# Kernel optimization log

Hardware: AMD Instinct MI355X
Metric: run time of the kernel (lower is better)

## Reference

```python
import jax, jax.numpy as jnp
import numpy as np

N, E, T = 20000, 320000, 64
INP, EMB, OUT = 128, 16, 3
HEADS, MSIZE, MDIM, KDIM, VDIM = 4, 1024, 128, 64, 64


def setup_inputs() -> dict:
    key = jax.random.key(0)
    ks = iter(jax.random.split(key, 64))

    def nrm(shape, s=0.05):
        return jax.random.normal(next(ks), shape, dtype=jnp.float32) * s

    return dict(
        x=jax.random.normal(next(ks), (N, INP), dtype=jnp.float32),
        edge_index=jax.random.randint(next(ks), (2, E), 0, N),
        index=5,
        inp_types=jax.random.randint(next(ks), (T,), 0, 4),
        log_return=jax.random.normal(next(ks), (T,), dtype=jnp.float32),
        # SAGEConv 1 (SoftmaxAggregation temp t1, lin_l/lin_r, bias=False)
        t1=jnp.ones((1, INP), jnp.float32),
        W1l=nrm((INP, 512)), W1r=nrm((INP, 512)),
        ln1g_w=jnp.ones((512,), jnp.float32), ln1g_b=jnp.zeros((512,), jnp.float32),
        # SAGEConv 2
        t2=jnp.ones((1, 512), jnp.float32),
        W2l=nrm((512, 256)), W2r=nrm((512, 256)),
        ln2g_w=jnp.ones((256,), jnp.float32), ln2g_b=jnp.zeros((256,), jnp.float32),
        # MemPooling(256,128,heads=4,num_clusters=1)
        mp_k=nrm((HEADS, 1, 256), 1.0),
        mp_conv=nrm((HEADS,), 0.5),            # Conv2d(heads,1,1,bias=False)
        mp_lin=nrm((256, 128)),                # Linear(in,out,bias=False)
        fxg_w=nrm((128, 256)), fxg_b=jnp.zeros((256,), jnp.float32),
        # PolicyNet head
        emb=nrm((4, EMB), 1.0),
        fk_w=nrm((256, KDIM)), fk_b=jnp.zeros((KDIM,), jnp.float32),
        fv_w=nrm((256, VDIM)), fv_b=jnp.zeros((VDIM,), jnp.float32),
        # MultiHeadMemory
        mem=nrm((HEADS, MSIZE, MDIM), 1.0),
        mfk_w=nrm((MDIM, KDIM)), mfk_b=jnp.zeros((KDIM,), jnp.float32),
        mfv_w=nrm((MDIM, VDIM)), mfv_b=jnp.zeros((VDIM,), jnp.float32),
        mfx_w=nrm((VDIM * HEADS, VDIM)), mfx_b=jnp.zeros((VDIM,), jnp.float32),
        f1_w=nrm((INP + EMB + 2 * VDIM + 1, 512)),
        n1_w=jnp.ones((512,), jnp.float32), n1_b=jnp.zeros((512,), jnp.float32),
        f2_w=nrm((512, 256)),
        n2_w=jnp.ones((256,), jnp.float32), n2_b=jnp.zeros((256,), jnp.float32),
        f3_w=nrm((256, OUT)), f3_b=jnp.zeros((OUT,), jnp.float32),
    )


def _forward(x, t1, W1l, W1r, ln1g_w, ln1g_b, t2, W2l, W2r, ln2g_w, ln2g_b,
             mp_k, mp_conv, mp_lin, fxg_w, fxg_b, emb, fk_w, fk_b, fv_w, fv_b,
             mem, mfk_w, mfk_b, mfv_w, mfv_b, mfx_w, mfx_b,
             f1_w, n1_w, n1_b, f2_w, n2_w, n2_b, f3_w, f3_b,
             log_return, edge_index, inp_types, index):
    n = x.shape[0]
    src, dst = edge_index[0], edge_index[1]

    def sage(h, t, Wl, Wr):
        hj = h[src]                                    # [E, C] gather
        gate = hj * t                                  # learned softmax temperature
        m = jax.ops.segment_max(gate, dst, num_segments=n)
        e = jnp.exp(gate - m[dst])                     # segment-stable softmax
        s = jax.ops.segment_sum(e, dst, num_segments=n)
        agg = jax.ops.segment_sum(hj * (e / s[dst]), dst, num_segments=n)
        return agg @ Wl + h @ Wr                       # SAGEConv, bias=False

    def graph_ln(h, w, b, eps=1e-5):                   # PyG LayerNorm, mode='graph'
        hc = h - jnp.mean(h)
        return hc / jnp.sqrt(jnp.mean(hc * hc) + eps) * w + b

    h = jax.nn.relu(graph_ln(sage(x, t1, W1l, W1r), ln1g_w, ln1g_b))
    h = jax.nn.relu(graph_ln(sage(h, t2, W2l, W2r), ln2g_w, ln2g_b))

    # MemPooling (single graph => B=1), tau=1: student-t kernel over sq. distances
    H, K, C = mp_k.shape
    kk = mp_k.reshape(H * K, C)
    d2 = jnp.maximum(jnp.sum(kk * kk, 1)[:, None] - 2.0 * (kk @ h.T)
                     + jnp.sum(h * h, 1)[None, :], 0.0)        # [H*K, N]
    dist = 1.0 / (1.0 + d2)
    dist = dist.reshape(H, K, n).transpose(0, 2, 1)[None]      # [1, H, N, K]
    S = dist / jnp.sum(dist, -1, keepdims=True)
    S = jax.nn.softmax(jnp.einsum('h,bhnk->bnk', mp_conv, S), axis=-1)  # [1, N, K]
    zp = jnp.einsum('bnk,nc->bkc', S, h)[:, 0, :]              # squeeze(1), K==1
    z = (zp @ mp_lin) @ fxg_w + fxg_b                          # [1, 256]

    q = jax.nn.softmax(z @ fk_w + fk_b, axis=-1)               # [1, key_dim]
    v = z @ fv_w + fv_b                                        # [1, val_dim]

    # MultiHeadMemory
    km = jax.nn.softmax(mem @ mfk_w + mfk_b, axis=-1)          # [H, M, key]
    vm = mem @ mfv_w + mfv_b                                   # [H, M, val]
    w = jax.nn.softmax(jnp.einsum('bk,hnk->bhn', q, km), axis=-1)
    mv = jnp.einsum('bhn,hnv->bhv', w, vm).reshape(q.shape[0], -1)
    m_out = mv @ mfx_w + mfx_b                                 # [1, val]

    zz = jnp.concatenate([v, m_out], axis=-1)                  # [1, 2*val]
    t_len = inp_types.shape[0]
    xi = jnp.broadcast_to(x[index][None, :], (t_len, x.shape[1]))
    zb = jnp.broadcast_to(zz, (t_len, zz.shape[1]))
    feat = jnp.concatenate([xi, emb[inp_types], log_return.reshape(-1, 1), zb], axis=-1)

    def ln(h2, w2, b2, eps=1e-5):                              # nn.LayerNorm (last dim)
        mu = jnp.mean(h2, -1, keepdims=True)
        hc = h2 - mu
        return hc / jnp.sqrt(jnp.mean(hc * hc, -1, keepdims=True) + eps) * w2 + b2

    h1 = jax.nn.relu(ln(feat @ f1_w, n1_w, n1_b))              # dropout = identity (eval)
    h2 = jax.nn.relu(ln(h1 @ f2_w, n2_w, n2_b))
    return jax.nn.softmax(h2 @ f3_w + f3_b, axis=-1)           # [T, out_dim]


def reference(x, edge_index, index, inp_types, log_return, t1, W1l, W1r, ln1g_w, ln1g_b,
              t2, W2l, W2r, ln2g_w, ln2g_b, mp_k, mp_conv, mp_lin, fxg_w, fxg_b, emb,
              fk_w, fk_b, fv_w, fv_b, mem, mfk_w, mfk_b, mfv_w, mfv_b, mfx_w, mfx_b,
              f1_w, n1_w, n1_b, f2_w, n2_w, n2_b, f3_w, f3_b):
    return _forward(x, t1, W1l, W1r, ln1g_w, ln1g_b, t2, W2l, W2r, ln2g_w, ln2g_b,
                    mp_k, mp_conv, mp_lin, fxg_w, fxg_b, emb, fk_w, fk_b, fv_w, fv_b,
                    mem, mfk_w, mfk_b, mfv_w, mfv_b, mfx_w, mfx_b,
                    f1_w, n1_w, n1_b, f2_w, n2_w, n2_b, f3_w, f3_b,
                    log_return, edge_index, inp_types, index)
```

## Files before the change

### kernel.cpp

```cpp
#include <hip/hip_runtime.h>

typedef __attribute__((ext_vector_type(8))) short bf16x8;
typedef __attribute__((ext_vector_type(8))) unsigned short ushort8_t;
typedef __attribute__((ext_vector_type(4))) float f32x4;

__device__ __forceinline__ unsigned short f2bf(float f) {
    unsigned int x = __float_as_uint(f);
    unsigned int r = x + 0x7fffu + ((x >> 16) & 1u);
    return (unsigned short)(r >> 16);
}
__device__ __forceinline__ float bf2f(unsigned short u) {
    return __uint_as_float(((unsigned int)u) << 16);
}
__device__ __forceinline__ float fexp2(float x) { return __builtin_amdgcn_exp2f(x); }

#define LOG2E 1.44269504089f

__global__ void count_kernel(const int* __restrict__ dst, int E, int* __restrict__ counts) {
    int i = blockIdx.x * 256 + threadIdx.x;
    if (i < E) atomicAdd(&counts[dst[i]], 1);
}

template <int CHUNK>
__global__ __launch_bounds__(1024) void scan_kernel(int* __restrict__ cnt,
                                                    int* __restrict__ off, int n) {
    __shared__ int s[1024];
    int tid = threadIdx.x;
    int base = tid * CHUNK;
    int loc[CHUNK];
    int sum = 0;
#pragma unroll
    for (int i = 0; i < CHUNK; ++i) {
        int idx = base + i;
        int v = 0;
        if (idx < n) { v = cnt[idx]; cnt[idx] = 0; }
        sum += v;
        loc[i] = sum;
    }
    s[tid] = sum;
    __syncthreads();
    for (int d = 1; d < 1024; d <<= 1) {
        int t = (tid >= d) ? s[tid - d] : 0;
        __syncthreads();
        s[tid] += t;
        __syncthreads();
    }
    int prev = (tid > 0) ? s[tid - 1] : 0;
    if (tid == 0) off[0] = 0;
#pragma unroll
    for (int i = 0; i < CHUNK; ++i) {
        int idx = base + i;
        if (idx < n) off[idx + 1] = prev + loc[i];
    }
}

__global__ void fill_kernel(const int* __restrict__ src, const int* __restrict__ dst, int E,
                            const int* __restrict__ off, int* __restrict__ cursor,
                            int* __restrict__ srcs) {
    int i = blockIdx.x * 256 + threadIdx.x;
    if (i < E) {
        int d = dst[i];
        int p = atomicAdd(&cursor[d], 1);
        srcs[off[d] + p] = src[i];
    }
}

__global__ __launch_bounds__(256) void cast_bf16(const float* __restrict__ in,
                                                 unsigned short* __restrict__ out, size_t n) {
    size_t stride = (size_t)gridDim.x * 256 * 4;
    for (size_t i = ((size_t)blockIdx.x * 256 + threadIdx.x) * 4; i < n; i += stride) {
        float4 v = *(const float4*)(in + i);
        ushort4 o;
        o.x = f2bf(v.x); o.y = f2bf(v.y); o.z = f2bf(v.z); o.w = f2bf(v.w);
        *(ushort4*)(out + i) = o;
    }
}

__global__ __launch_bounds__(256) void agg512(const unsigned short* __restrict__ h,
                                              const float* __restrict__ t,
                                              const int* __restrict__ off,
                                              const int* __restrict__ srcs,
                                              unsigned short* __restrict__ agg, int n) {
    int wid = threadIdx.x >> 6, lane = threadIdx.x & 63;
    int node = blockIdx.x * 4 + wid;
    if (node >= n) return;
    int beg = off[node], end = off[node + 1];
    int col = lane * 8;
    float tc[8], sE[8], sW[8];
#pragma unroll
    for (int i = 0; i < 8; ++i) { tc[i] = t[col + i] * LOG2E; sE[i] = 0.f; sW[i] = 0.f; }
#define P8(u)                                       \
    _Pragma("unroll") for (int i = 0; i < 8; ++i) { \
        float v = bf2f(u[i]);                       \
        float wv = fexp2(v * tc[i]);                \
        sE[i] += wv; sW[i] += v * wv;               \
    }
    int e = beg;
    for (; e + 2 <= end; e += 2) {
        int s0 = srcs[e], s1 = srcs[e + 1];
        ushort8_t u0 = *(const ushort8_t*)(h + (size_t)s0 * 512 + col);
        ushort8_t u1 = *(const ushort8_t*)(h + (size_t)s1 * 512 + col);
        P8(u0) P8(u1)
    }
    if (e < end) {
        int s0 = srcs[e];
        ushort8_t u0 = *(const ushort8_t*)(h + (size_t)s0 * 512 + col);
        P8(u0)
    }
#undef P8
    ushort8_t o;
#pragma unroll
    for (int i = 0; i < 8; ++i) o[i] = f2bf((end > beg) ? (sW[i] / sE[i]) : 0.f);
    *(ushort8_t*)(agg + (size_t)node * 512 + col) = o;
}

__global__ __launch_bounds__(256) void agg128(const unsigned short* __restrict__ h,
                                              const float* __restrict__ t,
                                              const int* __restrict__ off,
                                              const int* __restrict__ srcs,
                                              unsigned short* __restrict__ agg, int n) {
    int wid = threadIdx.x >> 6, lane = threadIdx.x & 63;
    int node = blockIdx.x * 4 + wid;
    if (node >= n) return;
    int beg = off[node], end = off[node + 1];
    int col = lane * 2;
    float t0 = t[col] * LOG2E, t1 = t[col + 1] * LOG2E;
    float e0 = 0.f, e1 = 0.f, w0 = 0.f, w1 = 0.f;
#define P2(u)                                          \
    {                                                  \
        float a = bf2f(u.x), b = bf2f(u.y);            \
        float xa = fexp2(a * t0), xb = fexp2(b * t1);  \
        e0 += xa; e1 += xb; w0 += a * xa; w1 += b * xb; \
    }
    int e = beg;
    for (; e + 4 <= end; e += 4) {
        ushort2 u0 = *(const ushort2*)(h + (size_t)srcs[e] * 128 + col);
        ushort2 u1 = *(const ushort2*)(h + (size_t)srcs[e + 1] * 128 + col);
        ushort2 u2 = *(const ushort2*)(h + (size_t)srcs[e + 2] * 128 + col);
        ushort2 u3 = *(const ushort2*)(h + (size_t)srcs[e + 3] * 128 + col);
        P2(u0) P2(u1) P2(u2) P2(u3)
    }
    for (; e < end; ++e) {
        ushort2 u0 = *(const ushort2*)(h + (size_t)srcs[e] * 128 + col);
        P2(u0)
    }
#undef P2
    ushort2 o;
    o.x = f2bf((end > beg) ? (w0 / e0) : 0.f);
    o.y = f2bf((end > beg) ? (w1 / e1) : 0.f);
    *(ushort2*)(agg + (size_t)node * 128 + col) = o;
}

__global__ void pack_w(const float* __restrict__ Wl, const float* __restrict__ Wr,
                       int K1, int K2, int N, unsigned short* __restrict__ Bt) {
    int idx = blockIdx.x * 256 + threadIdx.x;
    int Kc = K1 + K2;
    if (idx < N * Kc) {
        int n = idx / Kc;
        int k = idx - n * Kc;
        float v = (k < K1) ? Wl[(size_t)k * N + n] : Wr[(size_t)(k - K1) * N + n];
        Bt[idx] = f2bf(v);
    }
}

__global__ __launch_bounds__(512) void gemm_dual_mfma2(
    const unsigned short* __restrict__ A1, const unsigned short* __restrict__ A2,
    const unsigned short* __restrict__ Bt,
    unsigned short* __restrict__ Cb, double* __restrict__ part,
    int M, int N, int K1, int K2) {
    const int Kc = K1 + K2;
    __shared__ unsigned short As[128 * 40];
    __shared__ unsigned short Bs[256 * 40];
    __shared__ double rs[512], rs2[512];
    int tid = threadIdx.x;
    int lane = tid & 63, w = tid >> 6;
    int wm = w & 1, wn = w >> 1;
    int m0 = blockIdx.y * 128, n0 = blockIdx.x * 256;
    f32x4 acc[4][4] = {};
    int kg = lane >> 4, lr = lane & 15;

    for (int k0 = 0; k0 < Kc; k0 += 32) {
        const unsigned short* Asrc;
        int kk, Ksrc;
        if (k0 < K1) { Asrc = A1; kk = k0; Ksrc = K1; }
        else         { Asrc = A2; kk = k0 - K1; Ksrc = K2; }
        {
            int r = tid >> 2, ch = tid & 3;
            int gr = m0 + r;
            ushort8_t v = {0, 0, 0, 0, 0, 0, 0, 0};
            if (gr < M) v = *(const ushort8_t*)(Asrc + (size_t)gr * Ksrc + kk + ch * 8);
            *(ushort8_t*)&As[r * 40 + ch * 8] = v;
        }
#pragma unroll
        for (int it = 0; it < 2; ++it) {
            int idx = tid + it * 512;
            int r = idx >> 2, ch = idx & 3;
            const unsigned short* srcp = Bt + (size_t)(n0 + r) * Kc + k0 + ch * 8;
            *(ushort8_t*)&Bs[r * 40 + ch * 8] = *(const ushort8_t*)srcp;
        }
        __syncthreads();
        bf16x8 a[4], b[4];
#pragma unroll
        for (int i = 0; i < 4; ++i)
            a[i] = *(bf16x8*)&As[(wm * 64 + i * 16 + lr) * 40 + kg * 8];
#pragma unroll
        for (int j = 0; j < 4; ++j)
            b[j] = *(bf16x8*)&Bs[(wn * 64 + j * 16 + lr) * 40 + kg * 8];
#pragma unroll
        for (int i = 0; i < 4; ++i)
#pragma unroll
            for (int j = 0; j < 4; ++j)
                acc[i][j] = __builtin_amdgcn_mfma_f32_16x16x32_bf16(a[i], b[j], acc[i][j], 0, 0, 0);
        __syncthreads();
    }
    double s = 0, s2 = 0;
#pragma unroll
    for (int i = 0; i < 4; ++i) {
        int rbase = m0 + wm * 64 + i * 16 + kg * 4;
#pragma unroll
        for (int j = 0; j < 4; ++j) {
            int col = n0 + wn * 64 + j * 16 + lr;
#pragma unroll
            for (int reg = 0; reg < 4; ++reg) {
                int row = rbase + reg;
                if (row < M) {
                    float v = acc[i][j][reg];
                    Cb[(size_t)row * N + col] = f2bf(v);
                    s += v;
                    s2 += (double)v * v;
                }
            }
        }
    }
    rs[tid] = s;
    rs2[tid] = s2;
    __syncthreads();
    for (int d = 256; d; d >>= 1) {
        if (tid < d) { rs[tid] += rs[tid + d]; rs2[tid] += rs2[tid + d]; }
        __syncthreads();
    }
    if (tid == 0) {
        int bid = blockIdx.y * gridDim.x + blockIdx.x;
        part[bid * 2] = rs[0];
        part[bid * 2 + 1] = rs2[0];
    }
}

template <int C>
__global__ __launch_bounds__(256) void ln_relu_ip(unsigned short* __restrict__ z,
                                                  const float* __restrict__ w,
                                                  const float* __restrict__ b,
                                                  const double* __restrict__ part, int nb,
                                                  float invn, size_t n) {
    __shared__ float st[2];
    if (threadIdx.x < 64) {
        double s = 0, s2 = 0;
        for (int i = threadIdx.x; i < nb; i += 64) { s += part[2 * i]; s2 += part[2 * i + 1]; }
        for (int d = 32; d; d >>= 1) { s += __shfl_down(s, d); s2 += __shfl_down(s2, d); }
        if (threadIdx.x == 0) {
            float mu = (float)(s * invn);
            float var = (float)(s2 * invn) - mu * mu;
            st[0] = mu;
            st[1] = rsqrtf(var + 1e-5f);
        }
    }
    __syncthreads();
    float mu = st[0], inv = st[1];
    size_t stride = (size_t)gridDim.x * 256 * 4;
    for (size_t i = ((size_t)blockIdx.x * 256 + threadIdx.x) * 4; i < n; i += stride) {
        ushort4 v = *(const ushort4*)(z + i);
        int c = (int)(i & (C - 1));
        ushort4 o;
        o.x = f2bf(fmaxf((bf2f(v.x) - mu) * inv * w[c] + b[c], 0.f));
        o.y = f2bf(fmaxf((bf2f(v.y) - mu) * inv * w[c + 1] + b[c + 1], 0.f));
        o.z = f2bf(fmaxf((bf2f(v.z) - mu) * inv * w[c + 2] + b[c + 2], 0.f));
        o.w = f2bf(fmaxf((bf2f(v.w) - mu) * inv * w[c + 3] + b[c + 3], 0.f));
        *(ushort4*)(z + i) = o;
    }
}

__global__ __launch_bounds__(256) void colsum_t(const unsigned short* __restrict__ h2,
                                                float* __restrict__ cspartT, int n) {
    __shared__ float red[8 * 256];
    int tid = threadIdx.x;
    int cg = tid & 31;
    int rl = tid >> 5;
    int rows_per = (n + gridDim.x - 1) / gridDim.x;
    int r0 = blockIdx.x * rows_per;
    int r1 = min(n, r0 + rows_per);
    int c8 = cg * 8;
    float acc[8] = {};
    for (int r = r0 + rl; r < r1; r += 8) {
        ushort8_t u = *(const ushort8_t*)(h2 + (size_t)r * 256 + c8);
#pragma unroll
        for (int i = 0; i < 8; ++i) acc[i] += bf2f(u[i]);
    }
#pragma unroll
    for (int i = 0; i < 8; ++i) red[rl * 256 + c8 + i] = acc[i];
    __syncthreads();
    float s = 0;
#pragma unroll
    for (int r = 0; r < 8; ++r) s += red[r * 256 + tid];
    cspartT[tid * 64 + blockIdx.x] = s;
}

__global__ __launch_bounds__(256) void zqv_kernel(const float* __restrict__ cspartT,
                                                  const float* __restrict__ mp_lin,
                                                  const float* __restrict__ fxg_w,
                                                  const float* __restrict__ fxg_b,
                                                  const float* __restrict__ fk_w,
                                                  const float* __restrict__ fk_b,
                                                  const float* __restrict__ fv_w,
                                                  const float* __restrict__ fv_b,
                                                  float* __restrict__ qv) {
    __shared__ float zp_s[256], u_s[128], z_s[256], ql_s[64];
    __shared__ float part_s[1024];
    int tid = threadIdx.x;
    {
        float s = 0;
        const float* p = cspartT + tid * 64;
#pragma unroll
        for (int i = 0; i < 16; ++i) {
            float4 v = *(const float4*)(p + i * 4);
            s += v.x + v.y + v.z + v.w;
        }
        zp_s[tid] = s;
    }
    __syncthreads();
    {
        int og = tid & 31, kc = tid >> 5;
        int j4 = og * 4;
        f32x4 a = {0.f, 0.f, 0.f, 0.f};
        for (int ci = 0; ci < 32; ++ci) {
            int c = kc * 32 + ci;
            float4 w = *(const float4*)(mp_lin + (size_t)c * 128 + j4);
            float zc = zp_s[c];
            a[0] += zc * w.x; a[1] += zc * w.y; a[2] += zc * w.z; a[3] += zc * w.w;
        }
#pragma unroll
        for (int i = 0; i < 4; ++i) part_s[kc * 128 + j4 + i] = a[i];
    }
    __syncthreads();
    if (tid < 128) {
        float s = 0;
#pragma unroll
        for (int kc = 0; kc < 8; ++kc) s += part_s[kc * 128 + tid];
        u_s[tid] = s;
    }
    __syncthreads();
    {
        int og = tid & 63, kc = tid >> 6;
        int j4 = og * 4;
        f32x4 a = {0.f, 0.f, 0.f, 0.f};
        for (int ci = 0; ci < 32; ++ci) {
            int c = kc * 32 + ci;
            float4 w = *(const float4*)(fxg_w + (size_t)c * 256 + j4);
            float uc = u_s[c];
            a[0] += uc * w.x; a[1] += uc * w.y; a[2] += uc * w.z; a[3] += uc * w.w;
        }
#pragma unroll
        for (int i = 0; i < 4; ++i) part_s[kc * 256 + j4 + i] = a[i];
    }
    __syncthreads();
    {
        float s = fxg_b[tid];
#pragma unroll
        for (int kc = 0; kc < 4; ++kc) s += part_s[kc * 256 + tid];
        z_s[tid] = s;
    }
    __syncthreads();
    {
        int og = tid & 15, kc = tid >> 4;
        int j4 = og * 4;
        f32x4 a = {0.f, 0.f, 0.f, 0.f};
        for (int ci = 0; ci < 16; ++ci) {
            int c = kc * 16 + ci;
            float4 w = *(const float4*)(fk_w + (size_t)c * 64 + j4);
            float zc = z_s[c];
            a[0] += zc * w.x; a[1] += zc * w.y; a[2] += zc * w.z; a[3] += zc * w.w;
        }
#pragma unroll
        for (int i = 0; i < 4; ++i) part_s[kc * 64 + j4 + i] = a[i];
    }
    __syncthreads();
    if (tid < 64) {
        float s = fk_b[tid];
#pragma unroll
        for (int kc = 0; kc < 16; ++kc) s += part_s[kc * 64 + tid];
        ql_s[tid] = s;
    }
    __syncthreads();
    {
        int og = tid & 15, kc = tid >> 4;
        int j4 = og * 4;
        f32x4 a = {0.f, 0.f, 0.f, 0.f};
        for (int ci = 0; ci < 16; ++ci) {
            int c = kc * 16 + ci;
            float4 w = *(const float4*)(fv_w + (size_t)c * 64 + j4);
            float zc = z_s[c];
            a[0] += zc * w.x; a[1] += zc * w.y; a[2] += zc * w.z; a[3] += zc * w.w;
        }
#pragma unroll
        for (int i = 0; i < 4; ++i) part_s[kc * 64 + j4 + i] = a[i];
    }
    __syncthreads();
    if (tid < 64) {
        float mx = ql_s[tid];
        for (int d = 32; d; d >>= 1) mx = fmaxf(mx, __shfl_xor(mx, d));
        float e = __expf(ql_s[tid] - mx);
        float s = e;
        for (int d = 32; d; d >>= 1) s += __shfl_xor(s, d);
        qv[tid] = e / s;
        float vv = fv_b[tid];
#pragma unroll
        for (int kc = 0; kc < 16; ++kc) vv += part_s[kc * 64 + tid];
        qv[64 + tid] = vv;
    }
}

__global__ __launch_bounds__(256) void mem_kv_logit(const float* __restrict__ mem,
                                                    const float* __restrict__ mfk_w,
                                                    const float* __restrict__ mfk_b,
                                                    const float* __restrict__ mfv_w,
                                                    const float* __restrict__ mfv_b,
                                                    const float* __restrict__ qv,
                                                    float* __restrict__ logits,
                                                    float* __restrict__ vm) {
    __shared__ float rows[4][128];
    __shared__ float qs[64];
    int tid = threadIdx.x;
    int r0 = blockIdx.x * 4;
    if (tid < 64) qs[tid] = qv[tid];
    for (int i = tid; i < 512; i += 256) rows[i >> 7][i & 127] = mem[(size_t)r0 * 128 + i];
    __syncthreads();
    int lr = tid >> 6;
    int lane = tid & 63;
    const float* row = rows[lr];
    float kl = mfk_b[lane], vl = mfv_b[lane];
#pragma unroll 8
    for (int c = 0; c < 128; ++c) {
        float rv = row[c];
        kl += rv * mfk_w[c * 64 + lane];
        vl += rv * mfv_w[c * 64 + lane];
    }
    float mx = kl;
    for (int d = 32; d; d >>= 1) mx = fmaxf(mx, __shfl_xor(mx, d));
    float e = __expf(kl - mx);
    float s = e;
    for (int d = 32; d; d >>= 1) s += __shfl_xor(s, d);
    float kval = e / s;
    float wl = kval * qs[lane];
    for (int d = 32; d; d >>= 1) wl += __shfl_xor(wl, d);
    size_t gr = (size_t)(r0 + lr);
    if (lane == 0) logits[gr] = wl;
    vm[gr * 64 + lane] = vl;
}

__global__ __launch_bounds__(256) void attend_part(const float* __restrict__ logits,
                                                   const float* __restrict__ vm,
                                                   float* __restrict__ part) {
    int b = blockIdx.x;
    int h = b >> 4;
    int s0 = (b & 15) * 64;
    int tid = threadIdx.x;
    __shared__ float els[64];
    __shared__ float pr[4][64];
    __shared__ float lmax_s, lsum_s;
    if (tid < 64) {
        float lg = logits[h * 1024 + s0 + tid];
        float m = lg;
        for (int d = 32; d; d >>= 1) m = fmaxf(m, __shfl_xor(m, d));
        float e = __expf(lg - m);
        els[tid] = e;
        float s = e;
        for (int d = 32; d; d >>= 1) s += __shfl_xor(s, d);
        if (tid == 0) { lmax_s = m; lsum_s = s; }
    }
    __syncthreads();
    int dd = tid & 63, g = tid >> 6;
    float acc = 0;
    for (int s = g; s < 64; s += 4)
        acc += els[s] * vm[((size_t)h * 1024 + s0 + s) * 64 + dd];
    pr[g][dd] = acc;
    __syncthreads();
    if (tid < 64) {
        float pv = pr[0][tid] + pr[1][tid] + pr[2][tid] + pr[3][tid];
        part[b * 66 + 2 + tid] = pv;
        if (tid == 0) { part[b * 66] = lmax_s; part[b * 66 + 1] = lsum_s; }
    }
}

__global__ __launch_bounds__(256) void attend_final(const float* __restrict__ part,
                                                    const float* __restrict__ mfx_w,
                                                    const float* __restrict__ mfx_b,
                                                    float* __restrict__ m_out) {
    __shared__ float mv[256];
    __shared__ float part_s[1024];
    int tid = threadIdx.x;
    int h = tid >> 6, dd = tid & 63;
    float gmax = -1e30f;
#pragma unroll
    for (int p = 0; p < 16; ++p) gmax = fmaxf(gmax, part[(h * 16 + p) * 66]);
    float total = 0.f, acc = 0.f;
#pragma unroll
    for (int p = 0; p < 16; ++p) {
        float sc = __expf(part[(h * 16 + p) * 66] - gmax);
        total += part[(h * 16 + p) * 66 + 1] * sc;
        acc += part[(h * 16 + p) * 66 + 2 + dd] * sc;
    }
    mv[h * 64 + dd] = acc / total;
    __syncthreads();
    {
        int og = tid & 15, kc = tid >> 4;
        int j4 = og * 4;
        f32x4 a = {0.f, 0.f, 0.f, 0.f};
        for (int ci = 0; ci < 16; ++ci) {
            int c = kc * 16 + ci;
            float4 w = *(const float4*)(mfx_w + (size_t)c * 64 + j4);
            float mc = mv[c];
            a[0] += mc * w.x; a[1] += mc * w.y; a[2] += mc * w.z; a[3] += mc * w.w;
        }
#pragma unroll
        for (int i = 0; i < 4; ++i) part_s[kc * 64 + j4 + i] = a[i];
    }
    __syncthreads();
    if (tid < 64) {
        float s = mfx_b[tid];
#pragma unroll
        for (int kc = 0; kc < 16; ++kc) s += part_s[kc * 64 + tid];
        m_out[tid] = s;
    }
}

__device__ __forceinline__ float block_sum_256(float v, float* red) {
    int tid = threadIdx.x;
    red[tid] = v;
    __syncthreads();
    for (int d = 128; d; d >>= 1) { if (tid < d) red[tid] += red[tid + d]; __syncthreads(); }
    float r = red[0];
    __syncthreads();
    return r;
}

__global__ __launch_bounds__(256) void head_kernel(
    const float* __restrict__ x, const int* __restrict__ index_p,
    const int* __restrict__ inp_types, const float* __restrict__ log_return,
    const float* __restrict__ emb, const float* __restrict__ qv,
    const float* __restrict__ m_out, const float* __restrict__ f1_w,
    const float* __restrict__ n1_w, const float* __restrict__ n1_b,
    const float* __restrict__ f2_w, const float* __restrict__ n2_w,
    const float* __restrict__ n2_b, const float* __restrict__ f3_w,
    const float* __restrict__ f3_b, float* __restrict__ out) {
    __shared__ float feat[273];
    __shared__ float h1[512];
    __shared__ float h2[256];
    __shared__ float red[256];
    __shared__ float l3[3];
    int r = blockIdx.x, tid = threadIdx.x;
    int idx = index_p[0];
    for (int i = tid; i < 273; i += 256) {
        float val;
        if (i < 128) val = x[(size_t)idx * 128 + i];
        else if (i < 144) val = emb[inp_types[r] * 16 + (i - 128)];
        else if (i == 144) val = log_return[r];
        else if (i < 209) val = qv[64 + (i - 145)];
        else val = m_out[i - 209];
        feat[i] = val;
    }
    __syncthreads();
    float a0 = 0, a1 = 0;
    for (int c = 0; c < 273; ++c) {
        float f = feat[c];
        a0 += f * f1_w[c * 512 + tid];
        a1 += f * f1_w[c * 512 + tid + 256];
    }
    float mu = block_sum_256(a0 + a1, red) / 512.f;
    float c0 = a0 - mu, c1 = a1 - mu;
    float var = block_sum_256(c0 * c0 + c1 * c1, red) / 512.f;
    float inv = rsqrtf(var + 1e-5f);
    h1[tid] = fmaxf(c0 * inv * n1_w[tid] + n1_b[tid], 0.f);
    h1[tid + 256] = fmaxf(c1 * inv * n1_w[tid + 256] + n1_b[tid + 256], 0.f);
    __syncthreads();
    float b0 = 0;
    for (int c = 0; c < 512; ++c) b0 += h1[c] * f2_w[c * 256 + tid];
    float mu2 = block_sum_256(b0, red) / 256.f;
    float cc = b0 - mu2;
    float var2 = block_sum_256(cc * cc, red) / 256.f;
    float inv2 = rsqrtf(var2 + 1e-5f);
    h2[tid] = fmaxf(cc * inv2 * n2_w[tid] + n2_b[tid], 0.f);
    __syncthreads();
    if (tid < 3) {
        float a = f3_b[tid];
        for (int c = 0; c < 256; ++c) a += h2[c] * f3_w[c * 3 + tid];
        l3[tid] = a;
    }
    __syncthreads();
    if (tid < 3) {
        float mx = fmaxf(l3[0], fmaxf(l3[1], l3[2]));
        float s = __expf(l3[0] - mx) + __expf(l3[1] - mx) + __expf(l3[2] - mx);
        out[r * 3 + tid] = __expf(l3[tid] - mx) / s;
    }
}

extern "C" void kernel_launch(void* const* d_in, const int* in_sizes, int n_in,
                              void* d_out, int out_size, void* d_ws, size_t ws_size,
                              hipStream_t stream) {
    const float* x = (const float*)d_in[0];
    const int* ei = (const int*)d_in[1];
    const int* index_p = (const int*)d_in[2];
    const int* inp_types = (const int*)d_in[3];
    const float* log_return = (const float*)d_in[4];
    const float* t1 = (const float*)d_in[5];
    const float* W1l = (const float*)d_in[6];
    const float* W1r = (const float*)d_in[7];
    const float* ln1g_w = (const float*)d_in[8];
    const float* ln1g_b = (const float*)d_in[9];
    const float* t2 = (const float*)d_in[10];
    const float* W2l = (const float*)d_in[11];
    const float* W2r = (const float*)d_in[12];
    const float* ln2g_w = (const float*)d_in[13];
    const float* ln2g_b = (const float*)d_in[14];
    const float* mp_lin = (const float*)d_in[17];
    const float* fxg_w = (const float*)d_in[18];
    const float* fxg_b = (const float*)d_in[19];
    const float* emb = (const float*)d_in[20];
    const float* fk_w = (const float*)d_in[21];
    const float* fk_b = (const float*)d_in[22];
    const float* fv_w = (const float*)d_in[23];
    const float* fv_b = (const float*)d_in[24];
    const float* mem = (const float*)d_in[25];
    const float* mfk_w = (const float*)d_in[26];
    const float* mfk_b = (const float*)d_in[27];
    const float* mfv_w = (const float*)d_in[28];
    const float* mfv_b = (const float*)d_in[29];
    const float* mfx_w = (const float*)d_in[30];
    const float* mfx_b = (const float*)d_in[31];
    const float* f1_w = (const float*)d_in[32];
    const float* n1_w = (const float*)d_in[33];
    const float* n1_b = (const float*)d_in[34];
    const float* f2_w = (const float*)d_in[35];
    const float* n2_w = (const float*)d_in[36];
    const float* n2_b = (const float*)d_in[37];
    const float* f3_w = (const float*)d_in[38];
    const float* f3_b = (const float*)d_in[39];
    float* out = (float*)d_out;

    int n = in_sizes[0] / 128;
    int E = in_sizes[1] / 2;
    int T = in_sizes[3];
    const int* src = ei;
    const int* dst = ei + E;

    char* w = (char*)d_ws;
    auto alloc = [&](size_t bytes) {
        char* p = w;
        w += (bytes + 255) & ~(size_t)255;
        return p;
    };
    int* counts = (int*)alloc((size_t)n * 4);
    int* off = (int*)alloc((size_t)(n + 1) * 4);
    int* srcs = (int*)alloc((size_t)E * 4);
    unsigned short* xb = (unsigned short*)alloc((size_t)n * 128 * 2);
    unsigned short* agg1b = (unsigned short*)alloc((size_t)n * 128 * 2);
    unsigned short* z1b = (unsigned short*)alloc((size_t)n * 512 * 2);
    unsigned short* agg2b = (unsigned short*)alloc((size_t)n * 512 * 2);
    unsigned short* z2b = (unsigned short*)alloc((size_t)n * 256 * 2);
    double* partd = (double*)alloc(1024 * 2 * 8);
    float* cspartT = (float*)alloc(256 * 64 * 4);
    float* qv = (float*)alloc(128 * 4);
    float* logits = (float*)alloc((size_t)4 * 1024 * 4);
    float* vm = (float*)alloc((size_t)4 * 1024 * 64 * 4);
    float* apart = (float*)alloc(64 * 66 * 4);
    float* m_out = (float*)alloc(64 * 4);
    unsigned short* Bt1 = (unsigned short*)alloc((size_t)512 * 256 * 2);
    unsigned short* Bt2 = (unsigned short*)alloc((size_t)256 * 1024 * 2);

    int nblk_e = (E + 255) / 256;
    int mblk = (n + 127) / 128;

    hipMemsetAsync(counts, 0, (size_t)n * 4, stream);
    count_kernel<<<nblk_e, 256, 0, stream>>>(dst, E, counts);
    scan_kernel<20><<<1, 1024, 0, stream>>>(counts, off, n);
    fill_kernel<<<nblk_e, 256, 0, stream>>>(src, dst, E, off, counts, srcs);

    pack_w<<<(512 * 256 + 255) / 256, 256, 0, stream>>>(W1l, W1r, 128, 128, 512, Bt1);
    pack_w<<<(256 * 1024 + 255) / 256, 256, 0, stream>>>(W2l, W2r, 512, 512, 256, Bt2);
    cast_bf16<<<1024, 256, 0, stream>>>(x, xb, (size_t)n * 128);

    agg128<<<(n + 3) / 4, 256, 0, stream>>>(xb, t1, off, srcs, agg1b, n);
    gemm_dual_mfma2<<<dim3(2, mblk), 512, 0, stream>>>(agg1b, xb, Bt1, z1b, partd, n, 512, 128, 128);
    ln_relu_ip<512><<<1024, 256, 0, stream>>>(z1b, ln1g_w, ln1g_b, partd, 2 * mblk,
                                              1.0f / ((float)n * 512.f), (size_t)n * 512);

    agg512<<<(n + 3) / 4, 256, 0, stream>>>(z1b, t2, off, srcs, agg2b, n);
    gemm_dual_mfma2<<<dim3(1, mblk), 512, 0, stream>>>(agg2b, z1b, Bt2, z2b, partd, n, 256, 512, 512);
    ln_relu_ip<256><<<512, 256, 0, stream>>>(z2b, ln2g_w, ln2g_b, partd, mblk,
                                             1.0f / ((float)n * 256.f), (size_t)n * 256);

    colsum_t<<<64, 256, 0, stream>>>(z2b, cspartT, n);
    zqv_kernel<<<1, 256, 0, stream>>>(cspartT, mp_lin, fxg_w, fxg_b, fk_w, fk_b, fv_w, fv_b, qv);

    mem_kv_logit<<<1024, 256, 0, stream>>>(mem, mfk_w, mfk_b, mfv_w, mfv_b, qv, logits, vm);
    attend_part<<<64, 256, 0, stream>>>(logits, vm, apart);
    attend_final<<<1, 256, 0, stream>>>(apart, mfx_w, mfx_b, m_out);

    head_kernel<<<T, 256, 0, stream>>>(x, index_p, inp_types, log_return, emb, qv, m_out,
                                       f1_w, n1_w, n1_b, f2_w, n2_w, n2_b, f3_w, f3_b, out);
}
```

Before: 300.7 us.

## Fuse preprocessing kernels and fold final LayerNorm-ReLU into column sum

Merges the edge-count, x-to-bf16 cast and both weight-packing kernels into one prep kernel launched over the edge grid. It also removes the in-place LayerNorm+ReLU pass over z2 and applies the normalization and ReLU on the fly inside the column-sum reduction. Only the column sums are consumed downstream, so the separate read-modify-write of z2 is dropped. The cost is fewer launches and less memory traffic, in exchange for a prep kernel that has more work per thread and no bf16 rounding of the normalized values before summation.

After: 290.1 us. 3.5% less time.

```diff
diff --git a/kernel.cpp b/kernel.cpp
--- a/kernel.cpp
+++ b/kernel.cpp
@@ -16,9 +16,30 @@
 
 #define LOG2E 1.44269504089f
 
-__global__ void count_kernel(const int* __restrict__ dst, int E, int* __restrict__ counts) {
+__global__ __launch_bounds__(256) void prep_kernel(
+    const int* __restrict__ dst, int E, int* __restrict__ counts,
+    const float* __restrict__ x, unsigned short* __restrict__ xb, size_t nx4,
+    const float* __restrict__ W1l, const float* __restrict__ W1r, unsigned short* __restrict__ Bt1,
+    const float* __restrict__ W2l, const float* __restrict__ W2r, unsigned short* __restrict__ Bt2) {
     int i = blockIdx.x * 256 + threadIdx.x;
+    int total = gridDim.x * 256;
     if (i < E) atomicAdd(&counts[dst[i]], 1);
+    for (size_t j = i; j < nx4; j += total) {
+        float4 v = *(const float4*)(x + j * 4);
+        ushort4 o;
+        o.x = f2bf(v.x); o.y = f2bf(v.y); o.z = f2bf(v.z); o.w = f2bf(v.w);
+        *(ushort4*)(xb + j * 4) = o;
+    }
+    if (i < 512 * 256) {
+        int nn = i >> 8, k = i & 255;
+        float v = (k < 128) ? W1l[(size_t)k * 512 + nn] : W1r[(size_t)(k - 128) * 512 + nn];
+        Bt1[i] = f2bf(v);
+    }
+    if (i < 256 * 1024) {
+        int nn = i >> 10, k = i & 1023;
+        float v = (k < 512) ? W2l[(size_t)k * 256 + nn] : W2r[(size_t)(k - 512) * 256 + nn];
+        Bt2[i] = f2bf(v);
+    }
 }
 
 template <int CHUNK>
@@ -62,17 +83,6 @@
         int d = dst[i];
         int p = atomicAdd(&cursor[d], 1);
         srcs[off[d] + p] = src[i];
-    }
-}
-
-__global__ __launch_bounds__(256) void cast_bf16(const float* __restrict__ in,
-                                                 unsigned short* __restrict__ out, size_t n) {
-    size_t stride = (size_t)gridDim.x * 256 * 4;
-    for (size_t i = ((size_t)blockIdx.x * 256 + threadIdx.x) * 4; i < n; i += stride) {
-        float4 v = *(const float4*)(in + i);
-        ushort4 o;
-        o.x = f2bf(v.x); o.y = f2bf(v.y); o.z = f2bf(v.z); o.w = f2bf(v.w);
-        *(ushort4*)(out + i) = o;
     }
 }
 
@@ -151,18 +161,6 @@
     *(ushort2*)(agg + (size_t)node * 128 + col) = o;
 }
 
-__global__ void pack_w(const float* __restrict__ Wl, const float* __restrict__ Wr,
-                       int K1, int K2, int N, unsigned short* __restrict__ Bt) {
-    int idx = blockIdx.x * 256 + threadIdx.x;
-    int Kc = K1 + K2;
-    if (idx < N * Kc) {
-        int n = idx / Kc;
-        int k = idx - n * Kc;
-        float v = (k < K1) ? Wl[(size_t)k * N + n] : Wr[(size_t)(k - K1) * N + n];
-        Bt[idx] = f2bf(v);
-    }
-}
-
 __global__ __launch_bounds__(512) void gemm_dual_mfma2(
     const unsigned short* __restrict__ A1, const unsigned short* __restrict__ A2,
     const unsigned short* __restrict__ Bt,
@@ -279,21 +277,42 @@
     }
 }
 
-__global__ __launch_bounds__(256) void colsum_t(const unsigned short* __restrict__ h2,
-                                                float* __restrict__ cspartT, int n) {
+__global__ __launch_bounds__(256) void ln_colsum(const unsigned short* __restrict__ z2,
+                                                 const float* __restrict__ w,
+                                                 const float* __restrict__ b,
+                                                 const double* __restrict__ part, int nb,
+                                                 float invn, int n,
+                                                 float* __restrict__ cspartT) {
     __shared__ float red[8 * 256];
+    __shared__ float st[2];
     int tid = threadIdx.x;
+    if (tid < 64) {
+        double s = 0, s2 = 0;
+        for (int i = tid; i < nb; i += 64) { s += part[2 * i]; s2 += part[2 * i + 1]; }
+        for (int d = 32; d; d >>= 1) { s += __shfl_down(s, d); s2 += __shfl_down(s2, d); }
+        if (tid == 0) {
+            float mu = (float)(s * invn);
+            float var = (float)(s2 * invn) - mu * mu;
+            st[0] = mu;
+            st[1] = rsqrtf(var + 1e-5f);
+        }
+    }
+    __syncthreads();
+    float mu = st[0], inv = st[1];
     int cg = tid & 31;
     int rl = tid >> 5;
+    int c8 = cg * 8;
+    float lw[8], lb[8];
+#pragma unroll
+    for (int i = 0; i < 8; ++i) { lw[i] = w[c8 + i] * inv; lb[i] = b[c8 + i] - mu * inv * w[c8 + i]; }
     int rows_per = (n + gridDim.x - 1) / gridDim.x;
     int r0 = blockIdx.x * rows_per;
     int r1 = min(n, r0 + rows_per);
-    int c8 = cg * 8;
     float acc[8] = {};
     for (int r = r0 + rl; r < r1; r += 8) {
-        ushort8_t u = *(const ushort8_t*)(h2 + (size_t)r * 256 + c8);
-#pragma unroll
-        for (int i = 0; i < 8; ++i) acc[i] += bf2f(u[i]);
+        ushort8_t u = *(const ushort8_t*)(z2 + (size_t)r * 256 + c8);
+#pragma unroll
+        for (int i = 0; i < 8; ++i) acc[i] += fmaxf(bf2f(u[i]) * lw[i] + lb[i], 0.f);
     }
 #pragma unroll
     for (int i = 0; i < 8; ++i) red[rl * 256 + c8 + i] = acc[i];
@@ -679,13 +698,10 @@
     int mblk = (n + 127) / 128;
 
     hipMemsetAsync(counts, 0, (size_t)n * 4, stream);
-    count_kernel<<<nblk_e, 256, 0, stream>>>(dst, E, counts);
+    prep_kernel<<<nblk_e, 256, 0, stream>>>(dst, E, counts, x, xb, (size_t)n * 128 / 4,
+                                            W1l, W1r, Bt1, W2l, W2r, Bt2);
     scan_kernel<20><<<1, 1024, 0, stream>>>(counts, off, n);
     fill_kernel<<<nblk_e, 256, 0, stream>>>(src, dst, E, off, counts, srcs);
-
-    pack_w<<<(512 * 256 + 255) / 256, 256, 0, stream>>>(W1l, W1r, 128, 128, 512, Bt1);
-    pack_w<<<(256 * 1024 + 255) / 256, 256, 0, stream>>>(W2l, W2r, 512, 512, 256, Bt2);
-    cast_bf16<<<1024, 256, 0, stream>>>(x, xb, (size_t)n * 128);
 
     agg128<<<(n + 3) / 4, 256, 0, stream>>>(xb, t1, off, srcs, agg1b, n);
     gemm_dual_mfma2<<<dim3(2, mblk), 512, 0, stream>>>(agg1b, xb, Bt1, z1b, partd, n, 512, 128, 128);
@@ -694,10 +710,9 @@
 
     agg512<<<(n + 3) / 4, 256, 0, stream>>>(z1b, t2, off, srcs, agg2b, n);
     gemm_dual_mfma2<<<dim3(1, mblk), 512, 0, stream>>>(agg2b, z1b, Bt2, z2b, partd, n, 256, 512, 512);
-    ln_relu_ip<256><<<512, 256, 0, stream>>>(z2b, ln2g_w, ln2g_b, partd, mblk,
-                                             1.0f / ((float)n * 256.f), (size_t)n * 256);
-
-    colsum_t<<<64, 256, 0, stream>>>(z2b, cspartT, n);
+
+    ln_colsum<<<64, 256, 0, stream>>>(z2b, ln2g_w, ln2g_b, partd, mblk,
+                                      1.0f / ((float)n * 256.f), n, cspartT);
     zqv_kernel<<<1, 256, 0, stream>>>(cspartT, mp_lin, fxg_w, fxg_b, fk_w, fk_b, fv_w, fv_b, qv);
 
     mem_kv_logit<<<1024, 256, 0, stream>>>(mem, mfk_w, mfk_b, mfv_w, mfv_b, qv, logits, vm);
```
